# Kernel optimization log

Measured on AMD Instinct MI355X. Metric: run time of the kernel, lower is better.

## Reference

```python
import jax, jax.numpy as jnp
import numpy as np

D = 64          # embedding_dim
B = 1024        # batch (queries)
R = 128         # num_relations
N = 100000      # num_nodes
E = 6400000     # num_edges


def setup_inputs() -> dict:
    key = jax.random.key(0)
    ks = jax.random.split(key, 16)
    inp = {
        "relation_embeddings": jax.random.normal(ks[0], (B, R, D), dtype=jnp.float32),
        "query_rels": jax.random.randint(ks[1], (B,), 0, R),
        "query_entities": jax.random.randint(ks[2], (B,), 0, N),
        "edge_index": jax.random.randint(ks[3], (2, E), 0, N),
        "edge_type": jax.random.randint(ks[4], (E,), 0, R),
        "num_nodes": N,
        # feature_extractor: Linear(2D+4 -> D), ReLU, Linear(D -> D//2), ReLU
        "W1": jax.random.normal(ks[5], (2 * D + 4, D), dtype=jnp.float32) * 0.05,
        "b1": jnp.zeros((D,), dtype=jnp.float32),
        "W2": jax.random.normal(ks[6], (D, D // 2), dtype=jnp.float32) * 0.05,
        "b2": jnp.zeros((D // 2,), dtype=jnp.float32),
        # gate_network: Linear(D//2 -> D//4), ReLU, Linear(D//4 -> 1), Sigmoid
        "Wg1": jax.random.normal(ks[7], (D // 2, D // 4), dtype=jnp.float32) * 0.05,
        "bg1": jnp.zeros((D // 4,), dtype=jnp.float32),
        "Wg2": jax.random.normal(ks[8], (D // 4, 1), dtype=jnp.float32) * 0.05,
        "bg2": jnp.full((1,), 0.85, dtype=jnp.float32),
    }
    return inp


def reference(relation_embeddings, query_rels, query_entities, edge_index,
              edge_type, num_nodes, W1, b1, W2, b2, Wg1, bg1, Wg2, bg2):
    b, r, d = relation_embeddings.shape
    e = edge_type.shape[0]
    e_f = jnp.float32(e)
    src, dst = edge_index[0], edge_index[1]
    # count self-loop edges once (matches boolean OR mask in torch code)
    not_loop = (src != dst).astype(jnp.float32)

    # --- graph statistics (vectorized replacement of per-query masks) ---
    rel_counts = jnp.zeros((r,), jnp.float32).at[edge_type].add(1.0)          # [R]
    rel_freq_norm = jnp.minimum(rel_counts[query_rels] / e_f, 1.0)            # [B]

    deg = (jnp.zeros((num_nodes,), jnp.float32)
           .at[src].add(1.0).at[dst].add(not_loop))                           # [N]
    deg_q = deg[query_entities]                                               # [B]
    entity_degree_norm = jnp.minimum(deg_q / e_f, 1.0)

    density = jnp.minimum(e_f / jnp.float32(num_nodes * num_nodes), 1.0)
    stats = jnp.stack([rel_freq_norm, entity_degree_norm, rel_freq_norm,
                       jnp.full_like(rel_freq_norm, density)], axis=-1)       # [B,4]

    # --- query relation embedding ---
    rel_emb = relation_embeddings[jnp.arange(b), query_rels]                  # [B,D]

    # --- entity embedding = mean of relation embeddings over incident edges ---
    # per-node histogram of incident edge types (self loops counted once)
    hist = (jnp.zeros((num_nodes, r), jnp.float32)
            .at[src, edge_type].add(1.0)
            .at[dst, edge_type].add(not_loop))                                # [N,R]
    Mq = hist[query_entities]                                                 # [B,R]
    ent_sum = jnp.einsum('br,brd->bd', Mq, relation_embeddings)               # [B,D]
    entity_emb = ent_sum / jnp.maximum(deg_q, 1.0)[:, None]                   # zeros if deg==0

    # --- gated MLP ---
    feat = jnp.concatenate([rel_emb, entity_emb, stats], axis=-1)             # [B,2D+4]
    h = jax.nn.relu(feat @ W1 + b1)
    h = jax.nn.relu(h @ W2 + b2)
    g = jax.nn.relu(h @ Wg1 + bg1)
    gate = jax.nn.sigmoid(g @ Wg2 + bg2)[:, 0]                                # [B]
    return gate
```

## Files before the change

### kernel.cpp

```cpp
#include <hip/hip_runtime.h>
#include <math.h>


#define NNODES 100000
#define NWORDS ((NNODES + 31) / 32)
#define NWP    (((NWORDS + 3) / 4) * 4)
#define RR     128
#define DD     64
#define FF     (2 * DD + 4)
#define E4C    1600000
#define EDGE_BLOCKS 2048
#define EDGE_THREADS 256
#define NTC    (EDGE_BLOCKS * EDGE_THREADS)
#define HITCAP 512
#define SETUP_BLOCKS 256

__global__ void zero_kernel(int4* __restrict__ p, int n4)
{
    int i = blockIdx.x * blockDim.x + threadIdx.x;
    int stride = gridDim.x * blockDim.x;
    int4 z = make_int4(0, 0, 0, 0);
    for (int k = i; k < n4; k += stride) p[k] = z;
}

__global__ void __launch_bounds__(1024)
setup_kernel(const int* __restrict__ qents, int B,
             unsigned* __restrict__ gmask, int* __restrict__ gbase,
             const int* __restrict__ etype, int E,
             int* __restrict__ relcnt)
{
    int t = threadIdx.x;
    if (blockIdx.x != 0) {
        __shared__ int s_cnt[RR];
        if (t < RR) s_cnt[t] = 0;
        __syncthreads();
        int ne4 = E >> 2;
        const int4* et4 = (const int4*)etype;
        int i = (blockIdx.x - 1) * 1024 + t;
        int stride = (SETUP_BLOCKS - 1) * 1024;
        for (int k = i; k < ne4; k += stride) {
            int4 ty = et4[k];
            atomicAdd(&s_cnt[ty.x], 1);
            atomicAdd(&s_cnt[ty.y], 1);
            atomicAdd(&s_cnt[ty.z], 1);
            atomicAdd(&s_cnt[ty.w], 1);
        }
        if (blockIdx.x == 1) {
            for (int e = (ne4 << 2) + t; e < E; e += 1024)
                atomicAdd(&s_cnt[etype[e]], 1);
        }
        __syncthreads();
        if (t < RR) {
            int c = s_cnt[t];
            if (c) atomicAdd(&relcnt[t], c);
        }
        return;
    }
    __shared__ unsigned s_mask[NWP];
    __shared__ int s_wsum[16], s_wbase[16];
    for (int k = t; k < NWP; k += 1024) s_mask[k] = 0u;
    __syncthreads();
    for (int b = t; b < B; b += 1024) {
        int e = qents[b];
        atomicOr(&s_mask[e >> 5], 1u << (e & 31));
    }
    __syncthreads();
    int w0 = t * 4;
    int pc[4]; int sum = 0;
#pragma unroll
    for (int k = 0; k < 4; ++k) {
        int w = w0 + k;
        unsigned mm = (w < NWP) ? s_mask[w] : 0u;
        pc[k] = __popc(mm);
        sum += pc[k];
    }
    int lane = t & 63, wid = t >> 6;
    int incl = sum;
#pragma unroll
    for (int off = 1; off < 64; off <<= 1) {
        int v = __shfl_up(incl, off);
        if (lane >= off) incl += v;
    }
    if (lane == 63) s_wsum[wid] = incl;
    __syncthreads();
    if (t == 0) {
        int run = 0;
#pragma unroll
        for (int k = 0; k < 16; ++k) { s_wbase[k] = run; run += s_wsum[k]; }
    }
    __syncthreads();
    int base = s_wbase[wid] + incl - sum;
#pragma unroll
    for (int k = 0; k < 4; ++k) {
        int w = w0 + k;
        if (w < NWP) gbase[w] = base;
        base += pc[k];
    }
    for (int k = t; k < NWP; k += 1024) gmask[k] = s_mask[k];
}

static __device__ __forceinline__ void hitrec(
    int node, int e,
    const unsigned* s_mask, const int* __restrict__ gbase,
    unsigned* s_hnode, unsigned* s_hedge, int* s_hn,
    int* __restrict__ Mslot, const int* __restrict__ etype)
{
    unsigned w = s_mask[node >> 5];
    if ((w >> (node & 31)) & 1u) {
        int idx = atomicAdd(s_hn, 1);
        if (idx < HITCAP) {
            s_hnode[idx] = (unsigned)node;
            s_hedge[idx] = (unsigned)e;
        } else {
            int slot = gbase[node >> 5] + __popc(w & ((1u << (node & 31)) - 1u));
            atomicAdd(&Mslot[slot * RR + etype[e]], 1);
        }
    }
}

static __device__ __forceinline__ void edge4s(
    int4 s, int4 d, int i,
    const unsigned* s_mask, const int* __restrict__ gbase,
    unsigned* s_hnode, unsigned* s_hedge, int* s_hn,
    int* __restrict__ Mslot, const int* __restrict__ etype)
{
    int e = i * 4;
    hitrec(s.x, e + 0, s_mask, gbase, s_hnode, s_hedge, s_hn, Mslot, etype);
    if (s.x != d.x) hitrec(d.x, e + 0, s_mask, gbase, s_hnode, s_hedge, s_hn, Mslot, etype);
    hitrec(s.y, e + 1, s_mask, gbase, s_hnode, s_hedge, s_hn, Mslot, etype);
    if (s.y != d.y) hitrec(d.y, e + 1, s_mask, gbase, s_hnode, s_hedge, s_hn, Mslot, etype);
    hitrec(s.z, e + 2, s_mask, gbase, s_hnode, s_hedge, s_hn, Mslot, etype);
    if (s.z != d.z) hitrec(d.z, e + 2, s_mask, gbase, s_hnode, s_hedge, s_hn, Mslot, etype);
    hitrec(s.w, e + 3, s_mask, gbase, s_hnode, s_hedge, s_hn, Mslot, etype);
    if (s.w != d.w) hitrec(d.w, e + 3, s_mask, gbase, s_hnode, s_hedge, s_hn, Mslot, etype);
}

__global__ void __launch_bounds__(EDGE_THREADS, 8)
edge_kernel(const int* __restrict__ ei, const int* __restrict__ etype,
            int E, int E4,
            const unsigned* __restrict__ gmask, const int* __restrict__ gbase,
            int* __restrict__ Mslot)
{
    __shared__ __align__(16) unsigned s_mask[NWP];
    __shared__ unsigned s_hnode[HITCAP];
    __shared__ unsigned s_hedge[HITCAP];
    __shared__ int s_hn;
    int t = threadIdx.x;
    if (t == 0) s_hn = 0;
    const uint4* gm4 = (const uint4*)gmask;
    for (int i = t; i < NWP / 4; i += EDGE_THREADS)
        ((uint4*)s_mask)[i] = gm4[i];
    __syncthreads();

    int tid  = blockIdx.x * EDGE_THREADS + t;
    int nthr = gridDim.x * EDGE_THREADS;

    const int4* src4 = (const int4*)ei;
    const int4* dst4 = (const int4*)(ei + E);

    if (E4 == E4C && nthr == NTC) {
        int i0 = tid, i1 = tid + NTC, i2 = tid + 2 * NTC;
        int4 sa = src4[i0], da = dst4[i0];
        int4 sb = src4[i1], db = dst4[i1];
        int4 sc = src4[i2], dc = dst4[i2];
        edge4s(sa, da, i0, s_mask, gbase, s_hnode, s_hedge, &s_hn, Mslot, etype);
        edge4s(sb, db, i1, s_mask, gbase, s_hnode, s_hedge, &s_hn, Mslot, etype);
        edge4s(sc, dc, i2, s_mask, gbase, s_hnode, s_hedge, &s_hn, Mslot, etype);
        int i3 = tid + 3 * NTC;
        if (i3 < E4C) {
            int4 sd = src4[i3], dd = dst4[i3];
            edge4s(sd, dd, i3, s_mask, gbase, s_hnode, s_hedge, &s_hn, Mslot, etype);
        }
    } else {
        for (int i = tid; i < E4; i += nthr) {
            int4 s = src4[i], d = dst4[i];
            edge4s(s, d, i, s_mask, gbase, s_hnode, s_hedge, &s_hn, Mslot, etype);
        }
        for (int e = (E4 << 2) + tid; e < E; e += nthr) {
            int s = ei[e], d = ei[E + e];
            hitrec(s, e, s_mask, gbase, s_hnode, s_hedge, &s_hn, Mslot, etype);
            if (s != d)
                hitrec(d, e, s_mask, gbase, s_hnode, s_hedge, &s_hn, Mslot, etype);
        }
    }

    __syncthreads();
    int hn = s_hn; if (hn > HITCAP) hn = HITCAP;
    for (int i = t; i < hn; i += EDGE_THREADS) {
        int node = (int)s_hnode[i];
        int e    = (int)s_hedge[i];
        unsigned w = s_mask[node >> 5];
        int slot = gbase[node >> 5] + __popc(w & ((1u << (node & 31)) - 1u));
        atomicAdd(&Mslot[slot * RR + etype[e]], 1);
    }
}

__global__ void query_kernel(
    const float* __restrict__ RE,
    const int* __restrict__ qrels, const int* __restrict__ qents,
    const int* __restrict__ relcnt, const int* __restrict__ Mslot,
    const unsigned* __restrict__ gmask, const int* __restrict__ gbase,
    const float* __restrict__ W1, const float* __restrict__ b1,
    const float* __restrict__ W2, const float* __restrict__ b2,
    const float* __restrict__ Wg1, const float* __restrict__ bg1,
    const float* __restrict__ Wg2, const float* __restrict__ bg2,
    float* __restrict__ out, float e_f, float density)
{
    __shared__ float s_m[RR];
    __shared__ float s_part[256];
    __shared__ float s_feat[FF];
    __shared__ float s_h1[DD];
    __shared__ float s_h2[DD / 2];
    __shared__ float s_g[DD / 4];
    __shared__ int s_slot;

    int b = blockIdx.x;
    int t = threadIdx.x;
    int d = t & (DD - 1);
    int w = t >> 6;

    if (t == 0) {
        int e = qents[b];
        unsigned mm = gmask[e >> 5];
        s_slot = gbase[e >> 5] + __popc(mm & ((1u << (e & 31)) - 1u));
    }
    __syncthreads();
    int slot = s_slot;

    if (t < RR) s_m[t] = (float)Mslot[slot * RR + t];
    __syncthreads();

    const float* REb = RE + (size_t)b * RR * DD;
    float acc = 0.f;
#pragma unroll 8
    for (int r = w; r < RR; r += 4)
        acc = fmaf(s_m[r], REb[r * DD + d], acc);
    s_part[w * DD + d] = acc;
    __syncthreads();

    if (t < DD) {
        float ds = s_m[t] + s_m[t + DD];
#pragma unroll
        for (int off = 32; off > 0; off >>= 1) ds += __shfl_xor(ds, off);

        float ent = s_part[t] + s_part[DD + t] + s_part[2 * DD + t] + s_part[3 * DD + t];

        int qr = qrels[b];
        s_feat[t]      = REb[qr * DD + t];
        s_feat[DD + t] = ent / fmaxf(ds, 1.f);
        if (t == 0) {
            float rf = fminf((float)relcnt[qr] / e_f, 1.f);
            s_feat[2 * DD + 0] = rf;
            s_feat[2 * DD + 1] = fminf(ds / e_f, 1.f);
            s_feat[2 * DD + 2] = rf;
            s_feat[2 * DD + 3] = density;
        }
    }
    __syncthreads();

    {
        int c = t >> 6, n = t & 63;
        int i0 = c * 33;
        float a = 0.f;
#pragma unroll
        for (int k = 0; k < 33; ++k) {
            int i = i0 + k;
            a = fmaf(s_feat[i], W1[i * DD + n], a);
        }
        s_part[t] = a;
    }
    __syncthreads();
    if (t < DD) {
        float a = b1[t] + s_part[t] + s_part[64 + t] + s_part[128 + t] + s_part[192 + t];
        s_h1[t] = fmaxf(a, 0.f);
    }
    __syncthreads();

    {
        int c = t >> 5, n = t & 31;
        float a = 0.f;
#pragma unroll
        for (int k = 0; k < 8; ++k) {
            int i = c * 8 + k;
            a = fmaf(s_h1[i], W2[i * 32 + n], a);
        }
        s_part[t] = a;
    }
    __syncthreads();
    if (t < 32) {
        float a = b2[t];
#pragma unroll
        for (int c = 0; c < 8; ++c) a += s_part[c * 32 + t];
        s_h2[t] = fmaxf(a, 0.f);
    }
    __syncthreads();

    if (t < 16) {
        float a = bg1[t];
#pragma unroll
        for (int i = 0; i < 32; ++i) a = fmaf(s_h2[i], Wg1[i * 16 + t], a);
        s_g[t] = fmaxf(a, 0.f);
    }
    __syncthreads();

    if (t == 0) {
        float a = bg2[0];
#pragma unroll
        for (int i = 0; i < 16; ++i) a = fmaf(s_g[i], Wg2[i], a);
        out[b] = 1.f / (1.f + expf(-a));
    }
}

extern "C" void kernel_launch(void* const* d_in, const int* in_sizes, int n_in,
                              void* d_out, int out_size, void* d_ws, size_t ws_size,
                              hipStream_t stream)
{
    const float* RE    = (const float*)d_in[0];
    const int*   qrels = (const int*)d_in[1];
    const int*   qents = (const int*)d_in[2];
    const int*   ei    = (const int*)d_in[3];
    const int*   etype = (const int*)d_in[4];
    const float* W1  = (const float*)d_in[6];
    const float* b1  = (const float*)d_in[7];
    const float* W2  = (const float*)d_in[8];
    const float* b2  = (const float*)d_in[9];
    const float* Wg1 = (const float*)d_in[10];
    const float* bg1 = (const float*)d_in[11];
    const float* Wg2 = (const float*)d_in[12];
    const float* bg2 = (const float*)d_in[13];
    float* out = (float*)d_out;

    int B = in_sizes[1];
    int E = in_sizes[4];

    int* ws_i   = (int*)d_ws;
    int* Mslot  = ws_i;
    int* relcnt = Mslot + (size_t)B * RR;
    unsigned* mask = (unsigned*)(relcnt + RR);
    int* word_base = (int*)(mask + NWP);

    float e_f = (float)E;
    float density = fminf((float)E / ((float)NNODES * (float)NNODES), 1.f);

    int n4 = (B * RR + RR) / 4;
    zero_kernel<<<256, 256, 0, stream>>>((int4*)d_ws, n4);

    setup_kernel<<<SETUP_BLOCKS, 1024, 0, stream>>>(qents, B, mask, word_base,
                                                    etype, E, relcnt);

    int E4 = ((E & 3) == 0) ? (E >> 2) : 0;
    edge_kernel<<<EDGE_BLOCKS, EDGE_THREADS, 0, stream>>>(ei, etype, E, E4,
                                                          mask, word_base, Mslot);

    query_kernel<<<B, 256, 0, stream>>>(RE, qrels, qents, relcnt, Mslot,
                                        mask, word_base,
                                        W1, b1, W2, b2, Wg1, bg1, Wg2, bg2,
                                        out, e_f, density);
}
```

Before: 44.56 us.

## Fold workspace zeroing into setup kernel and replace relation-count atomics with partials

Removes the separate zero kernel launch by having the histogram blocks of the setup kernel zero the Mslot buffer. Per-block relation counts are written to a partial array instead of global atomics, and block 0 of the edge kernel reduces the partials into relcnt. The edge loop is also reordered to interleave loads with processing for more overlap. This saves a launch and global atomics, but adds a serial 255-element reduction in one block and relies on the zeroing covering all of Mslot before the edge kernel runs.

```diff
diff --git a/kernel.cpp b/kernel.cpp
--- a/kernel.cpp
+++ b/kernel.cpp
@@ -14,30 +14,25 @@
 #define NTC    (EDGE_BLOCKS * EDGE_THREADS)
 #define HITCAP 512
 #define SETUP_BLOCKS 256
-
-__global__ void zero_kernel(int4* __restrict__ p, int n4)
-{
-    int i = blockIdx.x * blockDim.x + threadIdx.x;
-    int stride = gridDim.x * blockDim.x;
-    int4 z = make_int4(0, 0, 0, 0);
-    for (int k = i; k < n4; k += stride) p[k] = z;
-}
+#define NHIST  (SETUP_BLOCKS - 1)
 
 __global__ void __launch_bounds__(1024)
 setup_kernel(const int* __restrict__ qents, int B,
              unsigned* __restrict__ gmask, int* __restrict__ gbase,
              const int* __restrict__ etype, int E,
-             int* __restrict__ relcnt)
+             int* __restrict__ relpart, int4* __restrict__ mz, int mz4)
 {
     int t = threadIdx.x;
     if (blockIdx.x != 0) {
         __shared__ int s_cnt[RR];
         if (t < RR) s_cnt[t] = 0;
         __syncthreads();
+        int zi = (blockIdx.x - 1) * 1024 + t;
+        if (zi < mz4) mz[zi] = make_int4(0, 0, 0, 0);
         int ne4 = E >> 2;
         const int4* et4 = (const int4*)etype;
         int i = (blockIdx.x - 1) * 1024 + t;
-        int stride = (SETUP_BLOCKS - 1) * 1024;
+        int stride = NHIST * 1024;
         for (int k = i; k < ne4; k += stride) {
             int4 ty = et4[k];
             atomicAdd(&s_cnt[ty.x], 1);
@@ -50,10 +45,7 @@
                 atomicAdd(&s_cnt[etype[e]], 1);
         }
         __syncthreads();
-        if (t < RR) {
-            int c = s_cnt[t];
-            if (c) atomicAdd(&relcnt[t], c);
-        }
+        if (t < RR) relpart[(blockIdx.x - 1) * RR + t] = s_cnt[t];
         return;
     }
     __shared__ unsigned s_mask[NWP];
@@ -139,7 +131,8 @@
 edge_kernel(const int* __restrict__ ei, const int* __restrict__ etype,
             int E, int E4,
             const unsigned* __restrict__ gmask, const int* __restrict__ gbase,
-            int* __restrict__ Mslot)
+            int* __restrict__ Mslot,
+            const int* __restrict__ relpart, int* __restrict__ relcnt)
 {
     __shared__ __align__(16) unsigned s_mask[NWP];
     __shared__ unsigned s_hnode[HITCAP];
@@ -147,6 +140,13 @@
     __shared__ int s_hn;
     int t = threadIdx.x;
     if (t == 0) s_hn = 0;
+
+    if (blockIdx.x == 0 && t < RR) {
+        int sum = 0;
+        for (int i = 0; i < NHIST; ++i) sum += relpart[i * RR + t];
+        relcnt[t] = sum;
+    }
+
     const uint4* gm4 = (const uint4*)gmask;
     for (int i = t; i < NWP / 4; i += EDGE_THREADS)
         ((uint4*)s_mask)[i] = gm4[i];
@@ -159,18 +159,18 @@
     const int4* dst4 = (const int4*)(ei + E);
 
     if (E4 == E4C && nthr == NTC) {
-        int i0 = tid, i1 = tid + NTC, i2 = tid + 2 * NTC;
-        int4 sa = src4[i0], da = dst4[i0];
-        int4 sb = src4[i1], db = dst4[i1];
-        int4 sc = src4[i2], dc = dst4[i2];
-        edge4s(sa, da, i0, s_mask, gbase, s_hnode, s_hedge, &s_hn, Mslot, etype);
-        edge4s(sb, db, i1, s_mask, gbase, s_hnode, s_hedge, &s_hn, Mslot, etype);
-        edge4s(sc, dc, i2, s_mask, gbase, s_hnode, s_hedge, &s_hn, Mslot, etype);
-        int i3 = tid + 3 * NTC;
-        if (i3 < E4C) {
-            int4 sd = src4[i3], dd = dst4[i3];
-            edge4s(sd, dd, i3, s_mask, gbase, s_hnode, s_hedge, &s_hn, Mslot, etype);
-        }
+        int i0 = tid, i1 = tid + NTC, i2 = tid + 2 * NTC, i3 = tid + 3 * NTC;
+        int4 s0 = src4[i0], d0 = dst4[i0];
+        int4 s1 = src4[i1], d1 = dst4[i1];
+        edge4s(s0, d0, i0, s_mask, gbase, s_hnode, s_hedge, &s_hn, Mslot, etype);
+        int4 s2 = src4[i2], d2 = dst4[i2];
+        edge4s(s1, d1, i1, s_mask, gbase, s_hnode, s_hedge, &s_hn, Mslot, etype);
+        bool has3 = (i3 < E4C);
+        int4 s3, d3;
+        if (has3) { s3 = src4[i3]; d3 = dst4[i3]; }
+        edge4s(s2, d2, i2, s_mask, gbase, s_hnode, s_hedge, &s_hn, Mslot, etype);
+        if (has3)
+            edge4s(s3, d3, i3, s_mask, gbase, s_hnode, s_hedge, &s_hn, Mslot, etype);
     } else {
         for (int i = tid; i < E4; i += nthr) {
             int4 s = src4[i], d = dst4[i];
@@ -338,19 +338,21 @@
     int* relcnt = Mslot + (size_t)B * RR;
     unsigned* mask = (unsigned*)(relcnt + RR);
     int* word_base = (int*)(mask + NWP);
+    int* relpart   = word_base + NWP;
 
     float e_f = (float)E;
     float density = fminf((float)E / ((float)NNODES * (float)NNODES), 1.f);
 
-    int n4 = (B * RR + RR) / 4;
-    zero_kernel<<<256, 256, 0, stream>>>((int4*)d_ws, n4);
+    int mz4 = (B * RR) / 4;
 
     setup_kernel<<<SETUP_BLOCKS, 1024, 0, stream>>>(qents, B, mask, word_base,
-                                                    etype, E, relcnt);
+                                                    etype, E, relpart,
+                                                    (int4*)Mslot, mz4);
 
     int E4 = ((E & 3) == 0) ? (E >> 2) : 0;
     edge_kernel<<<EDGE_BLOCKS, EDGE_THREADS, 0, stream>>>(ei, etype, E, E4,
-                                                          mask, word_base, Mslot);
+                                                          mask, word_base, Mslot,
+                                                          relpart, relcnt);
 
     query_kernel<<<B, 256, 0, stream>>>(RE, qrels, qents, relcnt, Mslot,
                                         mask, word_base,
```

Measured after the change: 46.50 us. +4.4%, slower.
